# Performance work log

Measured on AMD Instinct MI355X. Metric: run time of the kernel, lower is better.

## Reference

```python
import jax, jax.numpy as jnp
import numpy as np
from jax.scipy.linalg import block_diag

N_STATE, N_INPUT, HORIZON = 32, 16, 64


def setup_inputs() -> dict:
    key = jax.random.key(0)
    kA, kB, kC, kx = jax.random.split(key, 4)
    n_all = N_STATE + N_INPUT
    A = jax.random.normal(kA, (N_STATE, N_STATE), dtype=jnp.float32)
    B = jax.random.normal(kB, (N_STATE, N_INPUT), dtype=jnp.float32)
    Craw = jax.random.normal(kC, (HORIZON, n_all, n_all), dtype=jnp.float32)
    # symmetric positive-definite stage costs -> nonsingular KKT system
    C = jnp.einsum('tij,tkj->tik', Craw, Craw) / jnp.sqrt(jnp.float32(n_all)) \
        + jnp.eye(n_all, dtype=jnp.float32)
    x0 = jax.random.normal(kx, (N_STATE,), dtype=jnp.float32)
    return {"A": A, "B": B, "C": C, "T": HORIZON, "x0": x0}


def reference(A, B, C, T, x0):
    n_state = A.shape[0]
    n_input = B.shape[1]
    n_all = n_state + n_input
    dt = A.dtype

    # cost_mat: block-diagonal [n_all*T, n_all*T]
    cost_mat = block_diag(*C)

    # dynamics: [n_state*T, n_all*T]
    AB = jnp.concatenate((A, B), axis=1)              # [n_state, n_all]
    AB_blk = block_diag(*([AB] * (T - 1)))            # [(T-1)*n_state, (T-1)*n_all]
    dynamics = jnp.zeros((n_state * T, n_all * T), dtype=dt)
    dynamics = dynamics.at[:n_state, :n_state].set(jnp.eye(n_state, dtype=dt))
    dynamics = dynamics.at[n_state:n_state + (T - 1) * n_state,
                           :(T - 1) * n_all].set(AB_blk)
    # -I coupling entries: row n_state*t + i, col n_all*t + i, t=1..T-1
    t = jnp.arange(1, T)
    rows = (n_state * t)[:, None] + jnp.arange(n_state)[None, :]
    cols = (n_all * t)[:, None] + jnp.arange(n_state)[None, :]
    dynamics = dynamics.at[rows, cols].set(jnp.asarray(-1.0, dt))

    zero_mat = jnp.zeros((n_state * T, n_state * T), dtype=dt)
    full_mat = jnp.block([[cost_mat, dynamics.T],
                          [dynamics, zero_mat]])      # [(n_all+n_state)*T]^2

    # rhs: zeros except x0 at the start of the dynamics block
    sol = jnp.zeros(n_all * T + n_state * T, dtype=dt)
    sol = sol.at[n_all * T: n_all * T + n_state].set(x0)

    tau_mu = jnp.linalg.solve(full_mat, sol[:, None])[:, 0]
    tau_star = tau_mu[:n_all * T]
    mu_star = tau_mu[n_all * T:]
    return tau_star, mu_star
```

## Files before the change

kernel.cpp:

```cpp
#include <hip/hip_runtime.h>


namespace {

constexpr int NS  = 32;
constexpr int NI  = 16;
constexpr int NA  = 48;
constexpr int TT  = 64;
constexpr int NTH = 256;
constexpr int NBLK = 64;

using ull = unsigned long long;

__device__ __forceinline__ void fma4(float4& a, float s, const float4& b) {
  a.x += s * b.x; a.y += s * b.y; a.z += s * b.z; a.w += s * b.w;
}
__device__ __forceinline__ void fms4(float4& a, float s, const float4& b) {
  a.x -= s * b.x; a.y -= s * b.y; a.z -= s * b.z; a.w -= s * b.w;
}
__device__ __forceinline__ float dot4(const float4& a, const float4& b) {
  return a.x * b.x + a.y * b.y + a.z * b.z + a.w * b.w;
}
__device__ __forceinline__ float rdlane(float v, int l) {
  return __int_as_float(__builtin_amdgcn_readlane(__float_as_int(v), l));
}

__device__ __forceinline__ ull ald(const ull* p) {
  return __hip_atomic_load(p, __ATOMIC_RELAXED, __HIP_MEMORY_SCOPE_AGENT);
}
__device__ __forceinline__ void ast(ull* p, ull v) {
  __hip_atomic_store(p, v, __ATOMIC_RELAXED, __HIP_MEMORY_SCOPE_AGENT);
}
__device__ __forceinline__ ull pack2(float x, float y) {
  return (ull)__float_as_uint(x) | ((ull)__float_as_uint(y) << 32);
}
__device__ __forceinline__ float2 unpack2(ull v) {
  return make_float2(__uint_as_float((unsigned)v),
                     __uint_as_float((unsigned)(v >> 32)));
}
__device__ __forceinline__ float4 ald4(const ull* p) {
  ull lo = ald(p), hi = ald(p + 1);
  float2 a = unpack2(lo), b = unpack2(hi);
  return make_float4(a.x, a.y, b.x, b.y);
}
__device__ __forceinline__ void ast4(ull* p, const float4& v) {
  ast(p, pack2(v.x, v.y)); ast(p + 1, pack2(v.z, v.w));
}

__device__ __forceinline__ unsigned fld(const unsigned* f) {
  return __hip_atomic_load(f, __ATOMIC_RELAXED, __HIP_MEMORY_SCOPE_AGENT);
}
__device__ __forceinline__ void fst(unsigned* f) {
  __hip_atomic_store(f, 1u, __ATOMIC_RELAXED, __HIP_MEMORY_SCOPE_AGENT);
}
__device__ __forceinline__ void waitf(const unsigned* f) {
  if (threadIdx.x == 0)
    while (fld(f) == 0) __builtin_amdgcn_s_sleep(1);
  __syncthreads();
}
__device__ __forceinline__ void setf(unsigned* f) {
  asm volatile("s_waitcnt vmcnt(0)" ::: "memory");
  __syncthreads();
  if (threadIdx.x == 0) fst(f);
}

template<int K>
__device__ __forceinline__ void tile_outer(const float* Acol0, int lda,
                                           const float* Bcol0, int ldb,
                                           float4 acc[4]) {
  #pragma unroll
  for (int m = 0; m < K; ++m) {
    const float4 va = *(const float4*)(Acol0 + m * lda);
    const float4 vb = *(const float4*)(Bcol0 + m * ldb);
    fma4(acc[0], va.x, vb); fma4(acc[1], va.y, vb);
    fma4(acc[2], va.z, vb); fma4(acc[3], va.w, vb);
  }
}

template<int KQ>
__device__ __forceinline__ void tile_dot(const float* Arow0, int lda,
                                         const float* Brow0, int ldb,
                                         float acc[4][4]) {
  #pragma unroll
  for (int q = 0; q < KQ; ++q) {
    float4 va[4], vb[4];
    #pragma unroll
    for (int r = 0; r < 4; ++r) va[r] = *(const float4*)(Arow0 + r * lda + 4 * q);
    #pragma unroll
    for (int c = 0; c < 4; ++c) vb[c] = *(const float4*)(Brow0 + c * ldb + 4 * q);
    #pragma unroll
    for (int r = 0; r < 4; ++r)
      #pragma unroll
      for (int c = 0; c < 4; ++c) acc[r][c] += dot4(va[r], vb[c]);
  }
}

__device__ __forceinline__ float step_dot(const float4 m[8], float x) {
  float a0 = 0.f, a1 = 0.f, a2 = 0.f, a3 = 0.f;
  #pragma unroll
  for (int q = 0; q < 8; ++q) {
    a0 += rdlane(x, 4 * q + 0) * m[q].x;
    a1 += rdlane(x, 4 * q + 1) * m[q].y;
    a2 += rdlane(x, 4 * q + 2) * m[q].z;
    a3 += rdlane(x, 4 * q + 3) * m[q].w;
  }
  return (a0 + a1) + (a2 + a3);
}

__device__ __forceinline__ int nlev(int rm) {
  return (rm == TT - 1) ? 0 : (32 - __clz(TT - 1 - rm));
}

__global__ __launch_bounds__(NTH, 1) void lqr_all(
    const float* __restrict__ A, const float* __restrict__ Bm,
    const float* __restrict__ C, const float* __restrict__ x0,
    float* __restrict__ out,
    float* __restrict__ Sb0, float* __restrict__ Sb1,
    float* __restrict__ Mall, unsigned* __restrict__ flg) {
  __shared__ float sC [NA][NA];
  __shared__ float sAB[NS][NA];
  __shared__ float sRiST[NS][NI];
  __shared__ float sBRi [NS][NI];
  __shared__ float sAi[NS][NS], sCi[NS][NS], sJi[NS][NS];
  __shared__ float sAj[NS][NS], sCj[NS][NS], sJj[NS][NS];
  __shared__ float sAjT[NS][36];
  __shared__ float sV[NS][NS], sU[NS][NS];
  __shared__ float sY1[NS][NS], sY2[NS][NS], sW[NS][NS];
  __shared__ float sX[NS][NS], sZm[NS][NS];
  __shared__ float sG[NS][NA], sFu[NI][NA], sK[NI][NS], sK2[NI][NS];
  __shared__ float sXt0[NS], sXt1[NS];

  const int t = ((blockIdx.x & 7) << 3) | (blockIdx.x >> 3);
  const int tid = threadIdx.x, lane = tid & 63, wid = tid >> 6;
  unsigned* wr = flg;
  unsigned* rd = flg + 448;
  unsigned* mf = flg + 832;

  {
    const float* Ct = C + (size_t)t * NA * NA;
    for (int e = tid; e < NA * NA; e += NTH) sC[e / NA][e % NA] = Ct[e];
    for (int e = tid; e < NS * NA; e += NTH) {
      int i = e / NA, j = e % NA;
      sAB[i][j] = (j < NS) ? A[i * NS + j] : Bm[i * NI + (j - NS)];
    }
    __syncthreads();
    if (wid < 2 && lane < 48) {
      const int c = lane;
      float f[NI];
      if (c < NI) {
        #pragma unroll
        for (int i = 0; i < NI; ++i) f[i] = sC[NS + i][NS + c];
      } else {
        const int a = c - NI;
        if (wid == 0) {
          #pragma unroll
          for (int i = 0; i < NI; ++i) f[i] = sC[a][NS + i];
        } else {
          #pragma unroll
          for (int i = 0; i < NI; ++i) f[i] = sAB[a][NS + i];
        }
      }
      #pragma unroll
      for (int k = 0; k < NI; ++k) {
        float mi[NI];
        #pragma unroll
        for (int i = 0; i < NI; ++i) mi[i] = rdlane(f[i], k);
        const float inv = 1.0f / mi[k];
        f[k] *= inv;
        #pragma unroll
        for (int i = 0; i < NI; ++i) if (i != k) f[i] -= mi[i] * f[k];
      }
      if (c >= NI) {
        const int a = c - NI;
        float* D = (wid == 0) ? &sRiST[a][0] : &sBRi[a][0];
        #pragma unroll
        for (int i = 0; i < NI; ++i) D[i] = f[i];
      }
    }
    __syncthreads();
    ull* outA = (ull*)(Sb0 + (size_t)t * 3072);
    ull* outC = outA + 512;
    ull* outJ = outA + 1024;
    if (tid < 64) {
      const int a = tid >> 3, b = tid & 7;
      float acc[4][4];
      #pragma unroll
      for (int r = 0; r < 4; ++r)
        #pragma unroll
        for (int c = 0; c < 4; ++c) acc[r][c] = 0.f;
      tile_dot<4>(&sRiST[4 * a][0], NI, &sC[4 * b][NS], NA, acc);
      #pragma unroll
      for (int r = 0; r < 4; ++r) {
        const float4 q4 = *(const float4*)&sC[4 * a + r][4 * b];
        const float4 v = make_float4(q4.x - acc[r][0], q4.y - acc[r][1],
                                     q4.z - acc[r][2], q4.w - acc[r][3]);
        *(float4*)&sJi[4 * a + r][4 * b] = v;
        ast4(outJ + ((4 * a + r) * NS + 4 * b) / 2, v);
      }
    } else if (tid < 128) {
      const int q = tid - 64, a = q >> 3, b = q & 7;
      float acc[4][4];
      #pragma unroll
      for (int r = 0; r < 4; ++r)
        #pragma unroll
        for (int c = 0; c < 4; ++c) acc[r][c] = 0.f;
      tile_dot<4>(&sBRi[4 * a][0], NI, &sC[4 * b][NS], NA, acc);
      #pragma unroll
      for (int r = 0; r < 4; ++r) {
        const float4 a4 = *(const float4*)&sAB[4 * a + r][4 * b];
        const float4 v = make_float4(a4.x - acc[r][0], a4.y - acc[r][1],
                                     a4.z - acc[r][2], a4.w - acc[r][3]);
        *(float4*)&sAi[4 * a + r][4 * b] = v;
        ast4(outA + ((4 * a + r) * NS + 4 * b) / 2, v);
      }
    } else if (tid < 192) {
      const int q = tid - 128, a = q >> 3, b = q & 7;
      float acc[4][4];
      #pragma unroll
      for (int r = 0; r < 4; ++r)
        #pragma unroll
        for (int c = 0; c < 4; ++c) acc[r][c] = 0.f;
      tile_dot<4>(&sBRi[4 * a][0], NI, &sAB[4 * b][NS], NA, acc);
      #pragma unroll
      for (int r = 0; r < 4; ++r) {
        const float4 v = make_float4(acc[r][0], acc[r][1], acc[r][2], acc[r][3]);
        *(float4*)&sCi[4 * a + r][4 * b] = v;
        ast4(outC + ((4 * a + r) * NS + 4 * b) / 2, v);
      }
    }
  }
  setf(&wr[0 * 64 + t]);

  auto combine = [&]() {
    #pragma unroll
    for (int r = 0; r < 4; ++r) {
      const int e = tid + 256 * r, i = e >> 5, j = e & 31;
      sAjT[j][i] = sAj[i][j];
    }
    if (tid < 64) {
      const int a = tid >> 3, b = tid & 7;
      float4 acc[4] = {make_float4(0,0,0,0), make_float4(0,0,0,0),
                       make_float4(0,0,0,0), make_float4(0,0,0,0)};
      tile_outer<NS>(&sCi[0][4 * a], NS, &sJj[0][4 * b], NS, acc);
      if (a == b) { acc[0].x += 1.f; acc[1].y += 1.f; acc[2].z += 1.f; acc[3].w += 1.f; }
      #pragma unroll
      for (int r = 0; r < 4; ++r) *(float4*)&sX[4 * a + r][4 * b] = acc[r];
    }
    __syncthreads();
    if (wid < 2) {
      const int c = lane;
      float f[NS];
      if (c < NS) {
        #pragma unroll
        for (int i = 0; i < NS; ++i) f[i] = sX[i][c];
      } else if (wid == 0) {
        #pragma unroll
        for (int i = 0; i < NS; ++i) f[i] = sAi[i][c - NS];
      } else {
        #pragma unroll
        for (int i = 0; i < NS; ++i) f[i] = sCi[i][c - NS];
      }
      #pragma unroll
      for (int k = 0; k < NS; ++k) {
        float mi[NS];
        #pragma unroll
        for (int i = 0; i < NS; ++i) mi[i] = rdlane(f[i], k);
        const float inv = 1.0f / mi[k];
        f[k] *= inv;
        #pragma unroll
        for (int i = 0; i < NS; ++i) if (i != k) f[i] -= mi[i] * f[k];
      }
      if (c >= NS) {
        const int col = c - NS;
        if (wid == 0) {
          #pragma unroll
          for (int i = 0; i < NS; ++i) sV[i][col] = f[i];
        } else {
          #pragma unroll
          for (int i = 0; i < NS; ++i) sU[i][col] = f[i];
        }
      }
    }
    __syncthreads();
    if (tid < 192) {
      const int grp = tid >> 6, q = tid & 63, a = q >> 3, b = q & 7;
      float4 acc[4] = {make_float4(0,0,0,0), make_float4(0,0,0,0),
                       make_float4(0,0,0,0), make_float4(0,0,0,0)};
      if (grp == 0) {
        tile_outer<NS>(&sJj[0][4 * a], NS, &sV[0][4 * b], NS, acc);
        #pragma unroll
        for (int r = 0; r < 4; ++r) *(float4*)&sW[4 * a + r][4 * b] = acc[r];
      } else if (grp == 1) {
        tile_outer<NS>(&sAjT[0][4 * a], 36, &sV[0][4 * b], NS, acc);
        #pragma unroll
        for (int r = 0; r < 4; ++r) *(float4*)&sX[4 * a + r][4 * b] = acc[r];
      } else {
        tile_outer<NS>(&sAjT[0][4 * a], 36, &sU[0][4 * b], NS, acc);
        #pragma unroll
        for (int r = 0; r < 4; ++r) *(float4*)&sZm[4 * a + r][4 * b] = acc[r];
      }
    }
    __syncthreads();
    if (tid < 64) {
      const int a = tid >> 3, b = tid & 7;
      float4 acc[4] = {make_float4(0,0,0,0), make_float4(0,0,0,0),
                       make_float4(0,0,0,0), make_float4(0,0,0,0)};
      tile_outer<NS>(&sAi[0][4 * a], NS, &sW[0][4 * b], NS, acc);
      #pragma unroll
      for (int r = 0; r < 4; ++r) {
        const float4 j4 = *(const float4*)&sJi[4 * a + r][4 * b];
        acc[r].x += j4.x; acc[r].y += j4.y; acc[r].z += j4.z; acc[r].w += j4.w;
        *(float4*)&sY1[4 * a + r][4 * b] = acc[r];
      }
    } else if (tid < 128) {
      const int q = tid - 64, a = q >> 3, b = q & 7;
      float acc[4][4];
      #pragma unroll
      for (int r = 0; r < 4; ++r)
        #pragma unroll
        for (int c = 0; c < 4; ++c) acc[r][c] = 0.f;
      tile_dot<8>(&sZm[4 * a][0], NS, &sAj[4 * b][0], NS, acc);
      #pragma unroll
      for (int r = 0; r < 4; ++r) {
        const float4 c4 = *(const float4*)&sCj[4 * a + r][4 * b];
        *(float4*)&sY2[4 * a + r][4 * b] =
            make_float4(acc[r][0] + c4.x, acc[r][1] + c4.y,
                        acc[r][2] + c4.z, acc[r][3] + c4.w);
      }
    }
    __syncthreads();
    ((ull*)sAi)[tid] = ((const ull*)sX)[tid];
    ((ull*)sAi)[tid + 256] = ((const ull*)sX)[tid + 256];
    ((ull*)sCi)[tid] = ((const ull*)sY2)[tid];
    ((ull*)sCi)[tid + 256] = ((const ull*)sY2)[tid + 256];
    ((ull*)sJi)[tid] = ((const ull*)sY1)[tid];
    ((ull*)sJi)[tid + 256] = ((const ull*)sY1)[tid + 256];
    __syncthreads();
  };

  for (int l = 0; l < 6; ++l) {
    const int off = 1 << l;
    const int rm = t + off;
    if (rm < TT) {
      const int nlv = nlev(rm);
      const int v = (l < nlv) ? l : nlv;
      const float* Sin = (v & 1) ? Sb1 : Sb0;
      float* Sout = ((l + 1) & 1) ? Sb1 : Sb0;
      ull* Eo = (ull*)(Sout + (size_t)t * 3072);
      waitf(&wr[v * 64 + rm]);
      const ull* Ej = (const ull*)(Sin + (size_t)rm * 3072);
      {
        ull r0 = ald(Ej + tid),        r1 = ald(Ej + 256 + tid);
        ull r2 = ald(Ej + 512 + tid),  r3 = ald(Ej + 768 + tid);
        ull r4 = ald(Ej + 1024 + tid), r5 = ald(Ej + 1280 + tid);
        ((ull*)sAj)[tid] = r0; ((ull*)sAj)[tid + 256] = r1;
        ((ull*)sCj)[tid] = r2; ((ull*)sCj)[tid + 256] = r3;
        ((ull*)sJj)[tid] = r4; ((ull*)sJj)[tid + 256] = r5;
      }
      __syncthreads();
      if (v == l && tid == 0) fst(&rd[l * 64 + rm]);
      combine();
      if (l < 5) {
        if (l >= 1 && t >= (off >> 1)) waitf(&rd[(l - 1) * 64 + t]);
        ast(Eo + tid,        ((const ull*)sAi)[tid]);
        ast(Eo + 256 + tid,  ((const ull*)sAi)[tid + 256]);
        ast(Eo + 512 + tid,  ((const ull*)sCi)[tid]);
        ast(Eo + 768 + tid,  ((const ull*)sCi)[tid + 256]);
        ast(Eo + 1024 + tid, ((const ull*)sJi)[tid]);
        ast(Eo + 1280 + tid, ((const ull*)sJi)[tid + 256]);
        setf(&wr[(l + 1) * 64 + t]);
      }
    }
  }

  auto kmat = [&](int tau, bool hasP, float (*Pm)[NS], float (*Kd)[NS], bool wM) {
    const int ui = tid / 12, uk = tid - 12 * ui;
    float4 cr0 = make_float4(0,0,0,0), cr1 = make_float4(0,0,0,0);
    float4 cr2 = make_float4(0,0,0,0), cr3 = make_float4(0,0,0,0);
    if (tid < 48) {
      const float* Ct = C + (size_t)tau * NA * NA;
      cr0 = *(const float4*)&Ct[(NS + 4 * ui + 0) * NA + 4 * uk];
      cr1 = *(const float4*)&Ct[(NS + 4 * ui + 1) * NA + 4 * uk];
      cr2 = *(const float4*)&Ct[(NS + 4 * ui + 2) * NA + 4 * uk];
      cr3 = *(const float4*)&Ct[(NS + 4 * ui + 3) * NA + 4 * uk];
    }
    if (hasP) {
      if (tid < 96) {
        const int gi = tid / 12, gk = tid - 12 * gi;
        float4 acc[4] = {make_float4(0,0,0,0), make_float4(0,0,0,0),
                         make_float4(0,0,0,0), make_float4(0,0,0,0)};
        tile_outer<NS>(&Pm[0][4 * gi], NS, &sAB[0][4 * gk], NA, acc);
        #pragma unroll
        for (int r = 0; r < 4; ++r) *(float4*)&sG[4 * gi + r][4 * gk] = acc[r];
      }
    } else {
      for (int e = tid; e < NS * NA; e += NTH) sG[e / NA][e % NA] = 0.f;
    }
    __syncthreads();
    if (tid < 48) {
      float4 acc[4] = {cr0, cr1, cr2, cr3};
      tile_outer<NS>(&sAB[0][NS + 4 * ui], NA, &sG[0][4 * uk], NA, acc);
      #pragma unroll
      for (int r = 0; r < 4; ++r) *(float4*)&sFu[4 * ui + r][4 * uk] = acc[r];
    }
    __syncthreads();
    if (wid == 0) {
      const int col = (lane < 16) ? (NS + lane) : (lane - 16);
      float f[NI];
      #pragma unroll
      for (int i = 0; i < NI; ++i) f[i] = sFu[i][col];
      #pragma unroll
      for (int k = 0; k < NI; ++k) {
        float mi[NI];
        #pragma unroll
        for (int i = 0; i < NI; ++i) mi[i] = rdlane(f[i], k);
        const float inv = 1.0f / mi[k];
        f[k] *= inv;
        #pragma unroll
        for (int i = 0; i < NI; ++i) if (i != k) f[i] -= mi[i] * f[k];
      }
      if (lane >= 16 && lane < 48) {
        const int b = lane - 16;
        #pragma unroll
        for (int i = 0; i < NI; ++i) Kd[i][b] = f[i];
      }
    }
    __syncthreads();
    if (wM && tid < 64) {
      const int ma = tid >> 3, mb = tid & 7;
      float4 a0 = *(const float4*)&sAB[4 * ma + 0][4 * mb];
      float4 a1 = *(const float4*)&sAB[4 * ma + 1][4 * mb];
      float4 a2 = *(const float4*)&sAB[4 * ma + 2][4 * mb];
      float4 a3 = *(const float4*)&sAB[4 * ma + 3][4 * mb];
      #pragma unroll
      for (int q = 0; q < 4; ++q) {
        const float4 vf0 = *(const float4*)&sAB[4 * ma + 0][NS + 4 * q];
        const float4 vf1 = *(const float4*)&sAB[4 * ma + 1][NS + 4 * q];
        const float4 vf2 = *(const float4*)&sAB[4 * ma + 2][NS + 4 * q];
        const float4 vf3 = *(const float4*)&sAB[4 * ma + 3][NS + 4 * q];
        #pragma unroll
        for (int d = 0; d < 4; ++d) {
          const float4 vkk = *(const float4*)&Kd[4 * q + d][4 * mb];
          const float s0 = (d == 0) ? vf0.x : (d == 1) ? vf0.y : (d == 2) ? vf0.z : vf0.w;
          const float s1 = (d == 0) ? vf1.x : (d == 1) ? vf1.y : (d == 2) ? vf1.z : vf1.w;
          const float s2 = (d == 0) ? vf2.x : (d == 1) ? vf2.y : (d == 2) ? vf2.z : vf2.w;
          const float s3 = (d == 0) ? vf3.x : (d == 1) ? vf3.y : (d == 2) ? vf3.z : vf3.w;
          fms4(a0, s0, vkk); fms4(a1, s1, vkk); fms4(a2, s2, vkk); fms4(a3, s3, vkk);
        }
      }
      ull* Mt = (ull*)(Mall + (size_t)tau * NS * NS);
      ast4(Mt + (4 * ma + 0) * 16 + 2 * mb, a0);
      ast4(Mt + (4 * ma + 1) * 16 + 2 * mb, a1);
      ast4(Mt + (4 * ma + 2) * 16 + 2 * mb, a2);
      ast4(Mt + (4 * ma + 3) * 16 + 2 * mb, a3);
    }
    __syncthreads();
  };

  if (t >= 1) kmat(t - 1, true, sJi, sK, true);
  if (t == TT - 1) kmat(TT - 1, false, nullptr, sK2, false);
  setf(&mf[t]);

  {
    if (tid >= 1 && tid <= t) {
      while (fld(&mf[tid]) == 0) __builtin_amdgcn_s_sleep(1);
    }
    __syncthreads();
    if (wid == 0) {
      const int i = lane;
      if (i < NS) {
        const ull* Mg = (const ull*)Mall;
        float4 mA[8], mB[8];
        float x = x0[i];
        if (t == 1) sXt1[i] = x;
        if (t >= 1) {
          #pragma unroll
          for (int q = 0; q < 8; ++q) mA[q] = ald4(Mg + 0 * 512 + i * 16 + 2 * q);
        }
        if (t >= 2) {
          #pragma unroll
          for (int q = 0; q < 8; ++q) mB[q] = ald4(Mg + 1 * 512 + i * 16 + 2 * q);
        }
        for (int s = 0; s < t; s += 2) {
          x = step_dot(mA, x);
          if (s + 1 == t - 1) sXt1[i] = x;
          if (s + 2 < t) {
            #pragma unroll
            for (int q = 0; q < 8; ++q)
              mA[q] = ald4(Mg + (s + 2) * 512 + i * 16 + 2 * q);
          }
          if (s + 1 < t) {
            x = step_dot(mB, x);
            if (s + 2 == t - 1) sXt1[i] = x;
            if (s + 3 < t) {
              #pragma unroll
              for (int q = 0; q < 8; ++q)
                mB[q] = ald4(Mg + (s + 3) * 512 + i * 16 + 2 * q);
            }
          }
        }
        sXt0[i] = x;
        out[t * NA + i] = x;
      }
    }
    __syncthreads();
  }

  {
    if (t >= 1 && tid < NI) {
      const float4* Kr = (const float4*)&sK[tid][0];
      const float4* xr = (const float4*)sXt1;
      float acc = 0.f;
      #pragma unroll
      for (int q = 0; q < 8; ++q) acc += dot4(Kr[q], xr[q]);
      out[(t - 1) * NA + NS + tid] = -acc;
    } else if (tid >= NI && tid < NI + NS) {
      const int i = tid - NI;
      const float4* Pr = (const float4*)&sJi[i][0];
      const float4* xr = (const float4*)sXt0;
      float acc = 0.f;
      #pragma unroll
      for (int q = 0; q < 8; ++q) acc += dot4(Pr[q], xr[q]);
      out[NA * TT + t * NS + i] = (t == 0) ? -acc : acc;
    } else if (t == TT - 1 && tid >= 192 && tid < 192 + NI) {
      const int i = tid - 192;
      const float4* Kr = (const float4*)&sK2[i][0];
      const float4* xr = (const float4*)sXt0;
      float acc = 0.f;
      #pragma unroll
      for (int q = 0; q < 8; ++q) acc += dot4(Kr[q], xr[q]);
      out[(TT - 1) * NA + NS + i] = -acc;
    }
  }
}

}

extern "C" void kernel_launch(void* const* d_in, const int* in_sizes, int n_in,
                              void* d_out, int out_size, void* d_ws, size_t ws_size,
                              hipStream_t stream) {
  const float* A  = (const float*)d_in[0];
  const float* Bm = (const float*)d_in[1];
  const float* C  = (const float*)d_in[2];
  const float* x0 = (const float*)d_in[4];
  float* out = (float*)d_out;

  float* Sb0 = (float*)d_ws;
  float* Sb1 = Sb0 + (size_t)TT * 3072;
  float* Mall = Sb1 + (size_t)TT * 3072;
  unsigned* flg = (unsigned*)(Mall + (size_t)TT * NS * NS);

  hipMemsetAsync(flg, 0, 4096, stream);
  hipLaunchKernelGGL(lqr_all, dim3(NBLK), dim3(NTH), 0, stream,
                     A, Bm, C, x0, out, Sb0, Sb1, Mall, flg);
}
```

Baseline: 126.5 us.

## Compute neighbor's initial element locally to skip first-level cross-block exchange

Each block now also loads C for step t+1 and computes that step's initial (A,C,J) element itself, writing it straight into the j-side shared buffers. This removes the level-0 global-memory store, flag wait and load between blocks, plus the matching read-ack wait at level 1. Only block T-1 still publishes its initial element. The cost is duplicated factorization work and extra shared memory (a new scratch buffer aliased with sG/sFu, and sV/sU reused for the neighbor's intermediates).

```diff
diff --git a/kernel.cpp b/kernel.cpp
--- a/kernel.cpp
+++ b/kernel.cpp
@@ -118,6 +118,7 @@
     float* __restrict__ Sb0, float* __restrict__ Sb1,
     float* __restrict__ Mall, unsigned* __restrict__ flg) {
   __shared__ float sC [NA][NA];
+  __shared__ float sScr[NA * NA];
   __shared__ float sAB[NS][NA];
   __shared__ float sRiST[NS][NI];
   __shared__ float sBRi [NS][NI];
@@ -127,7 +128,7 @@
   __shared__ float sV[NS][NS], sU[NS][NS];
   __shared__ float sY1[NS][NS], sY2[NS][NS], sW[NS][NS];
   __shared__ float sX[NS][NS], sZm[NS][NS];
-  __shared__ float sG[NS][NA], sFu[NI][NA], sK[NI][NS], sK2[NI][NS];
+  __shared__ float sK[NI][NS], sK2[NI][NS];
   __shared__ float sXt0[NS], sXt1[NS];
 
   const int t = ((blockIdx.x & 7) << 3) | (blockIdx.x >> 3);
@@ -136,100 +137,112 @@
   unsigned* rd = flg + 448;
   unsigned* mf = flg + 832;
 
+  float (*sC2)[NA]    = (float(*)[NA])sScr;
+  float (*sRiST2)[NI] = (float(*)[NI])sV;
+  float (*sBRi2)[NI]  = (float(*)[NI])sU;
+
   {
     const float* Ct = C + (size_t)t * NA * NA;
     for (int e = tid; e < NA * NA; e += NTH) sC[e / NA][e % NA] = Ct[e];
+    if (t + 1 < TT) {
+      const float* Ct1 = C + (size_t)(t + 1) * NA * NA;
+      for (int e = tid; e < NA * NA; e += NTH) sC2[e / NA][e % NA] = Ct1[e];
+    }
     for (int e = tid; e < NS * NA; e += NTH) {
       int i = e / NA, j = e % NA;
       sAB[i][j] = (j < NS) ? A[i * NS + j] : Bm[i * NI + (j - NS)];
     }
     __syncthreads();
-    if (wid < 2 && lane < 48) {
-      const int c = lane;
-      float f[NI];
-      if (c < NI) {
-        #pragma unroll
-        for (int i = 0; i < NI; ++i) f[i] = sC[NS + i][NS + c];
-      } else {
-        const int a = c - NI;
-        if (wid == 0) {
-          #pragma unroll
-          for (int i = 0; i < NI; ++i) f[i] = sC[a][NS + i];
+    {
+      const int ew = wid >> 1, sub = wid & 1;
+      if ((ew == 0 || t + 1 < TT) && lane < 48) {
+        float (*Cm)[NA] = ew ? sC2 : sC;
+        const int c = lane;
+        float f[NI];
+        if (c < NI) {
+          #pragma unroll
+          for (int i = 0; i < NI; ++i) f[i] = Cm[NS + i][NS + c];
         } else {
-          #pragma unroll
-          for (int i = 0; i < NI; ++i) f[i] = sAB[a][NS + i];
-        }
-      }
-      #pragma unroll
-      for (int k = 0; k < NI; ++k) {
-        float mi[NI];
-        #pragma unroll
-        for (int i = 0; i < NI; ++i) mi[i] = rdlane(f[i], k);
-        const float inv = 1.0f / mi[k];
-        f[k] *= inv;
-        #pragma unroll
-        for (int i = 0; i < NI; ++i) if (i != k) f[i] -= mi[i] * f[k];
-      }
-      if (c >= NI) {
-        const int a = c - NI;
-        float* D = (wid == 0) ? &sRiST[a][0] : &sBRi[a][0];
-        #pragma unroll
-        for (int i = 0; i < NI; ++i) D[i] = f[i];
+          const int a = c - NI;
+          if (sub == 0) {
+            #pragma unroll
+            for (int i = 0; i < NI; ++i) f[i] = Cm[a][NS + i];
+          } else {
+            #pragma unroll
+            for (int i = 0; i < NI; ++i) f[i] = sAB[a][NS + i];
+          }
+        }
+        #pragma unroll
+        for (int k = 0; k < NI; ++k) {
+          float mi[NI];
+          #pragma unroll
+          for (int i = 0; i < NI; ++i) mi[i] = rdlane(f[i], k);
+          const float inv = 1.0f / mi[k];
+          f[k] *= inv;
+          #pragma unroll
+          for (int i = 0; i < NI; ++i) if (i != k) f[i] -= mi[i] * f[k];
+        }
+        if (c >= NI) {
+          const int a = c - NI;
+          float* D = (sub == 0) ? (ew ? &sRiST2[a][0] : &sRiST[a][0])
+                                : (ew ? &sBRi2[a][0]  : &sBRi[a][0]);
+          #pragma unroll
+          for (int i = 0; i < NI; ++i) D[i] = f[i];
+        }
       }
     }
     __syncthreads();
     ull* outA = (ull*)(Sb0 + (size_t)t * 3072);
     ull* outC = outA + 512;
     ull* outJ = outA + 1024;
-    if (tid < 64) {
-      const int a = tid >> 3, b = tid & 7;
+    const int nwork = (t + 1 < TT) ? 384 : 192;
+    for (int u = tid; u < nwork; u += NTH) {
+      const int grp = u >> 6, q = u & 63, a = q >> 3, b = q & 7;
+      const int ew = (grp >= 3) ? 1 : 0, g3 = grp - 3 * ew;
+      float (*Cm)[NA]    = ew ? sC2 : sC;
+      float (*RiSTm)[NI] = ew ? sRiST2 : sRiST;
+      float (*BRim)[NI]  = ew ? sBRi2 : sBRi;
       float acc[4][4];
       #pragma unroll
       for (int r = 0; r < 4; ++r)
         #pragma unroll
         for (int c = 0; c < 4; ++c) acc[r][c] = 0.f;
-      tile_dot<4>(&sRiST[4 * a][0], NI, &sC[4 * b][NS], NA, acc);
-      #pragma unroll
-      for (int r = 0; r < 4; ++r) {
-        const float4 q4 = *(const float4*)&sC[4 * a + r][4 * b];
-        const float4 v = make_float4(q4.x - acc[r][0], q4.y - acc[r][1],
-                                     q4.z - acc[r][2], q4.w - acc[r][3]);
-        *(float4*)&sJi[4 * a + r][4 * b] = v;
-        ast4(outJ + ((4 * a + r) * NS + 4 * b) / 2, v);
-      }
-    } else if (tid < 128) {
-      const int q = tid - 64, a = q >> 3, b = q & 7;
-      float acc[4][4];
-      #pragma unroll
-      for (int r = 0; r < 4; ++r)
-        #pragma unroll
-        for (int c = 0; c < 4; ++c) acc[r][c] = 0.f;
-      tile_dot<4>(&sBRi[4 * a][0], NI, &sC[4 * b][NS], NA, acc);
-      #pragma unroll
-      for (int r = 0; r < 4; ++r) {
-        const float4 a4 = *(const float4*)&sAB[4 * a + r][4 * b];
-        const float4 v = make_float4(a4.x - acc[r][0], a4.y - acc[r][1],
-                                     a4.z - acc[r][2], a4.w - acc[r][3]);
-        *(float4*)&sAi[4 * a + r][4 * b] = v;
-        ast4(outA + ((4 * a + r) * NS + 4 * b) / 2, v);
-      }
-    } else if (tid < 192) {
-      const int q = tid - 128, a = q >> 3, b = q & 7;
-      float acc[4][4];
-      #pragma unroll
-      for (int r = 0; r < 4; ++r)
-        #pragma unroll
-        for (int c = 0; c < 4; ++c) acc[r][c] = 0.f;
-      tile_dot<4>(&sBRi[4 * a][0], NI, &sAB[4 * b][NS], NA, acc);
-      #pragma unroll
-      for (int r = 0; r < 4; ++r) {
-        const float4 v = make_float4(acc[r][0], acc[r][1], acc[r][2], acc[r][3]);
-        *(float4*)&sCi[4 * a + r][4 * b] = v;
-        ast4(outC + ((4 * a + r) * NS + 4 * b) / 2, v);
-      }
-    }
-  }
-  setf(&wr[0 * 64 + t]);
+      if (g3 == 0) {
+        tile_dot<4>(&RiSTm[4 * a][0], NI, &Cm[4 * b][NS], NA, acc);
+        float (*dJ)[NS] = ew ? sJj : sJi;
+        #pragma unroll
+        for (int r = 0; r < 4; ++r) {
+          const float4 q4 = *(const float4*)&Cm[4 * a + r][4 * b];
+          const float4 v = make_float4(q4.x - acc[r][0], q4.y - acc[r][1],
+                                       q4.z - acc[r][2], q4.w - acc[r][3]);
+          *(float4*)&dJ[4 * a + r][4 * b] = v;
+          if (ew == 0 && t == TT - 1) ast4(outJ + ((4 * a + r) * NS + 4 * b) / 2, v);
+        }
+      } else if (g3 == 1) {
+        tile_dot<4>(&BRim[4 * a][0], NI, &Cm[4 * b][NS], NA, acc);
+        float (*dA)[NS] = ew ? sAj : sAi;
+        #pragma unroll
+        for (int r = 0; r < 4; ++r) {
+          const float4 a4 = *(const float4*)&sAB[4 * a + r][4 * b];
+          const float4 v = make_float4(a4.x - acc[r][0], a4.y - acc[r][1],
+                                       a4.z - acc[r][2], a4.w - acc[r][3]);
+          *(float4*)&dA[4 * a + r][4 * b] = v;
+          if (ew == 0 && t == TT - 1) ast4(outA + ((4 * a + r) * NS + 4 * b) / 2, v);
+        }
+      } else {
+        tile_dot<4>(&BRim[4 * a][0], NI, &sAB[4 * b][NS], NA, acc);
+        float (*dC)[NS] = ew ? sCj : sCi;
+        #pragma unroll
+        for (int r = 0; r < 4; ++r) {
+          const float4 v = make_float4(acc[r][0], acc[r][1], acc[r][2], acc[r][3]);
+          *(float4*)&dC[4 * a + r][4 * b] = v;
+          if (ew == 0 && t == TT - 1) ast4(outC + ((4 * a + r) * NS + 4 * b) / 2, v);
+        }
+      }
+    }
+  }
+  if (t == TT - 1) setf(&wr[0 * 64 + t]);
+  else __syncthreads();
 
   auto combine = [&]() {
     #pragma unroll
@@ -342,26 +355,27 @@
     const int off = 1 << l;
     const int rm = t + off;
     if (rm < TT) {
-      const int nlv = nlev(rm);
-      const int v = (l < nlv) ? l : nlv;
-      const float* Sin = (v & 1) ? Sb1 : Sb0;
-      float* Sout = ((l + 1) & 1) ? Sb1 : Sb0;
-      ull* Eo = (ull*)(Sout + (size_t)t * 3072);
-      waitf(&wr[v * 64 + rm]);
-      const ull* Ej = (const ull*)(Sin + (size_t)rm * 3072);
-      {
-        ull r0 = ald(Ej + tid),        r1 = ald(Ej + 256 + tid);
-        ull r2 = ald(Ej + 512 + tid),  r3 = ald(Ej + 768 + tid);
-        ull r4 = ald(Ej + 1024 + tid), r5 = ald(Ej + 1280 + tid);
-        ((ull*)sAj)[tid] = r0; ((ull*)sAj)[tid + 256] = r1;
-        ((ull*)sCj)[tid] = r2; ((ull*)sCj)[tid + 256] = r3;
-        ((ull*)sJj)[tid] = r4; ((ull*)sJj)[tid + 256] = r5;
-      }
-      __syncthreads();
-      if (v == l && tid == 0) fst(&rd[l * 64 + rm]);
+      if (l >= 1) {
+        const int nlv = nlev(rm);
+        const int v = (l < nlv) ? l : nlv;
+        const float* Sin = (v & 1) ? Sb1 : Sb0;
+        waitf(&wr[v * 64 + rm]);
+        const ull* Ej = (const ull*)(Sin + (size_t)rm * 3072);
+        {
+          ull r0 = ald(Ej + tid),        r1 = ald(Ej + 256 + tid);
+          ull r2 = ald(Ej + 512 + tid),  r3 = ald(Ej + 768 + tid);
+          ull r4 = ald(Ej + 1024 + tid), r5 = ald(Ej + 1280 + tid);
+          ((ull*)sAj)[tid] = r0; ((ull*)sAj)[tid + 256] = r1;
+          ((ull*)sCj)[tid] = r2; ((ull*)sCj)[tid + 256] = r3;
+          ((ull*)sJj)[tid] = r4; ((ull*)sJj)[tid + 256] = r5;
+        }
+        __syncthreads();
+        if (v == l && tid == 0) fst(&rd[l * 64 + rm]);
+      }
       combine();
       if (l < 5) {
-        if (l >= 1 && t >= (off >> 1)) waitf(&rd[(l - 1) * 64 + t]);
+        if (l >= 2 && t >= (off >> 1)) waitf(&rd[(l - 1) * 64 + t]);
+        ull* Eo = (ull*)((((l + 1) & 1) ? Sb1 : Sb0) + (size_t)t * 3072);
         ast(Eo + tid,        ((const ull*)sAi)[tid]);
         ast(Eo + 256 + tid,  ((const ull*)sAi)[tid + 256]);
         ast(Eo + 512 + tid,  ((const ull*)sCi)[tid]);
@@ -373,6 +387,8 @@
     }
   }
 
+  float (*sG)[NA]  = (float(*)[NA])sScr;
+  float (*sFu)[NA] = (float(*)[NA])(sScr + NS * NA);
   auto kmat = [&](int tau, bool hasP, float (*Pm)[NS], float (*Kd)[NS], bool wM) {
     const int ui = tid / 12, uk = tid - 12 * ui;
     float4 cr0 = make_float4(0,0,0,0), cr1 = make_float4(0,0,0,0);
```

Measured after the change: 127.4 us. No clear change (+0.7%).
